# Kernel optimization log

Measured on AMD Instinct MI355X. Metric: run time of the kernel, lower is better.

## Reference

```python
import jax, jax.numpy as jnp
import numpy as np

CHUNK = 1024
HEAD_DIM = 128

def setup_inputs() -> dict:
    key = jax.random.key(0)
    k1, k2, k3 = jax.random.split(key, 3)
    B, H, S, D = 2, 16, 4096, HEAD_DIM
    q = jax.random.normal(k1, (B, H, S, D), dtype=jnp.float32)
    k = jax.random.normal(k2, (B, H, S, D), dtype=jnp.float32)
    v = jax.random.normal(k3, (B, H, S, D), dtype=jnp.float32)
    return {"q": q, "k": k, "v": v}

def reference(q, k, v):
    # Faithful to the torch module INCLUDING its masking bug: for every chunk
    # the triu mask uses diagonal=1 in chunk-local coordinates, so chunk-local
    # query row i attends only keys j<=i, i.e. only the first CHUNK keys matter.
    B, H, S, D = q.shape
    scale = D ** (-0.5)
    n = S // CHUNK
    qc = q.reshape(B, H, n, CHUNK, D)           # [B,H,n,C,D]
    kc = k[:, :, :CHUNK, :]                      # [B,H,C,D]
    vc = v[:, :, :CHUNK, :]                      # [B,H,C,D]
    scores = jnp.einsum('bhnid,bhjd->bhnij', qc, kc) * scale  # [B,H,n,C,C]
    mask = jnp.triu(jnp.ones((CHUNK, CHUNK), dtype=bool), 1)   # j > i masked
    scores = jnp.where(mask, -jnp.inf, scores)
    probs = jax.nn.softmax(scores, axis=-1)
    out = jnp.einsum('bhnij,bhjd->bhnid', probs, vc)
    return out.reshape(B, H, S, D)
```

## Files before the change

kernel.cpp:

```cpp
#include <hip/hip_runtime.h>


typedef __attribute__((ext_vector_type(8))) short bfrag_t;
typedef __attribute__((ext_vector_type(16))) float f32x16;
typedef unsigned short u16;
typedef unsigned int   u32;

#define SEQ     4096
#define SCHUNK  1024
#define HD      128
#define NTILE   16
#define TILE_E  8192

__device__ __forceinline__ u16 f2bf(float f) {
    union { float f; unsigned u; } x; x.f = f;
    unsigned r = x.u + 0x7fffu + ((x.u >> 16) & 1u);
    return (u16)(r >> 16);
}

__global__ __launch_bounds__(256)
void mea_prep(const float* __restrict__ kg, const float* __restrict__ vg,
              u16* __restrict__ wsK, u16* __restrict__ wsV)
{
    const int tid  = threadIdx.x;
    const int tile = blockIdx.x;
    const int bh = tile >> 4, kt = tile & 15;
    const long gsrc = (long)bh * SEQ * HD + (long)kt * 64 * HD;
    const long gdst = (long)tile * TILE_E;

#pragma unroll
    for (int i = 0; i < 4; ++i) {
        int oid = i * 256 + tid;
        int j = oid >> 4, s = oid & 15;
        const float* kp = kg + gsrc + j * HD + s * 8;
        float4 a = *(const float4*)kp;
        float4 b = *(const float4*)(kp + 4);
        bfrag_t f;
        f[0]=f2bf(a.x); f[1]=f2bf(a.y); f[2]=f2bf(a.z); f[3]=f2bf(a.w);
        f[4]=f2bf(b.x); f[5]=f2bf(b.y); f[6]=f2bf(b.z); f[7]=f2bf(b.w);
        *(bfrag_t*)(wsK + gdst + j * 128 + ((s ^ (j & 15)) * 8)) = f;
    }
#pragma unroll
    for (int i = 0; i < 4; ++i) {
        int oid = i * 256 + tid;
        int jo = oid >> 7, d = oid & 127;
        const float* vp = vg + gsrc + jo * 8 * HD + d;
        bfrag_t f;
#pragma unroll
        for (int jj = 0; jj < 8; ++jj) f[jj] = f2bf(vp[jj * HD]);
        int d2 = d >> 1;
        int S  = (jo + ((d & 1) << 3)) ^ (d2 & 15);
        *(bfrag_t*)(wsV + gdst + d2 * 128 + S * 8) = f;
    }
}

__device__ __forceinline__ void gll16(const u16* g, u16* l) {
    __builtin_amdgcn_global_load_lds((const __attribute__((address_space(1))) u32*)g,
                                     (__attribute__((address_space(3))) u32*)l, 16, 0, 0);
}

__device__ __forceinline__ float tsum16(const f32x16& p) {
    float a0 = (p[0] + p[1]) + (p[2] + p[3]);
    float a1 = (p[4] + p[5]) + (p[6] + p[7]);
    float a2 = (p[8] + p[9]) + (p[10] + p[11]);
    float a3 = (p[12] + p[13]) + (p[14] + p[15]);
    return (a0 + a1) + (a2 + a3);
}

__device__ __forceinline__ void sm_cvt(f32x16& s, float& lsum, bfrag_t* pf) {
#pragma unroll
    for (int r = 0; r < 16; ++r) s[r] = exp2f(s[r]);
    lsum += tsum16(s);
    u32 W[8];
#pragma unroll
    for (int t2 = 0; t2 < 8; ++t2)
        asm("v_cvt_pk_bf16_f32 %0, %1, %2"
            : "=v"(W[t2]) : "v"(s[2 * t2]), "v"(s[2 * t2 + 1]));
#pragma unroll
    for (int u2 = 0; u2 < 2; ++u2) {
        u32 x0 = W[4 * u2 + 0], y0 = W[4 * u2 + 2];
        u32 x1 = W[4 * u2 + 1], y1 = W[4 * u2 + 3];
        asm("v_permlane32_swap_b32 %0, %1" : "+v"(x0), "+v"(y0));
        asm("v_permlane32_swap_b32 %0, %1" : "+v"(x1), "+v"(y1));
        union { u32 w[4]; bfrag_t f; } cvt;
        cvt.w[0] = x0; cvt.w[1] = x1; cvt.w[2] = y0; cvt.w[3] = y1;
        pf[u2] = cvt.f;
    }
}

__global__ __launch_bounds__(512, 2)
void mea_main(const float* __restrict__ qg, const u16* __restrict__ wsK,
              const u16* __restrict__ wsV, float* __restrict__ og)
{
    __shared__ __align__(16) u16 K_s[2][TILE_E];
    __shared__ __align__(16) u16 V_s[2][TILE_E];

    const int tid  = threadIdx.x;
    const int lane = tid & 63;
    const int wv   = tid >> 6;
    const int c31  = lane & 31;
    const int hi   = lane >> 5;
    const int ch   = wv & 3;
    const int h    = wv >> 2;

    const int x   = blockIdx.x & 7;
    const int idx = blockIdx.x >> 3;
    const int bh  = x * 4 + (idx & 3);
    const int p   = idx >> 2;

    const long bhrow = (long)bh * SEQ + (long)ch * SCHUNK + (long)h * 32;
    const u16* Kb = wsK + (long)bh * NTILE * TILE_E;
    const u16* Vb = wsV + (long)bh * NTILE * TILE_E;
    const int so   = wv * 1024 + lane * 8;
    const int ldsb = wv * 1024;
    const float qs = 0.12751723f;

#pragma unroll
    for (int c = 0; c < 2; ++c) {
        gll16(Kb + so + c * 512, &K_s[0][ldsb + c * 512]);
        gll16(Vb + so + c * 512, &V_s[0][ldsb + c * 512]);
    }

    int cur = 0;
    for (int seg = 0; seg < 2; ++seg) {
        const int qt = seg ? p : (15 - p);
        const int nt = qt + 1;
        const long rowbase = bhrow + (long)qt * 64;

        bfrag_t qf[8];
        {
            const float* qp = qg + (rowbase + c31) * HD + hi * 8;
#pragma unroll
            for (int ks = 0; ks < 8; ++ks) {
                float4 a = *(const float4*)(qp + ks * 16);
                float4 b = *(const float4*)(qp + ks * 16 + 4);
                bfrag_t f;
                f[0]=f2bf(a.x*qs); f[1]=f2bf(a.y*qs); f[2]=f2bf(a.z*qs); f[3]=f2bf(a.w*qs);
                f[4]=f2bf(b.x*qs); f[5]=f2bf(b.y*qs); f[6]=f2bf(b.z*qs); f[7]=f2bf(b.w*qs);
                qf[ks] = f;
            }
        }

        f32x16 oacc[4];
#pragma unroll
        for (int d = 0; d < 4; ++d)
#pragma unroll
            for (int i = 0; i < 16; ++i) oacc[d][i] = 0.f;
        float lsum = 0.f;

        for (int kt = 0; kt < nt; ++kt) {
            __syncthreads();

            if (kt + 1 < nt) {
                const long tb = (long)(kt + 1) * TILE_E;
#pragma unroll
                for (int c = 0; c < 2; ++c) {
                    gll16(Kb + tb + so + c * 512, &K_s[cur ^ 1][ldsb + c * 512]);
                    gll16(Vb + tb + so + c * 512, &V_s[cur ^ 1][ldsb + c * 512]);
                }
            } else if (seg == 0) {
#pragma unroll
                for (int c = 0; c < 2; ++c) {
                    gll16(Kb + so + c * 512, &K_s[cur ^ 1][ldsb + c * 512]);
                    gll16(Vb + so + c * 512, &V_s[cur ^ 1][ldsb + c * 512]);
                }
            }

            const bool diag = (kt == nt - 1);
            const bool do1  = !(diag && h == 0);
            bfrag_t pfA[2], pfB[2];

            {
                f32x16 s;
#pragma unroll
                for (int i = 0; i < 16; ++i) s[i] = 0.f;
                const u16* krow = &K_s[cur][c31 * 128];
                __builtin_amdgcn_s_setprio(1);
#pragma unroll
                for (int ks = 0; ks < 8; ++ks) {
                    int slot = (ks * 2 + hi) ^ (c31 & 15);
                    bfrag_t kf = *(const bfrag_t*)(krow + slot * 8);
                    s = __builtin_amdgcn_mfma_f32_32x32x16_bf16(kf, qf[ks], s, 0, 0, 0);
                }
                __builtin_amdgcn_s_setprio(0);
                if (diag && h == 0) {
#pragma unroll
                    for (int r = 0; r < 16; ++r) {
                        int crow = (r & 3) + 8 * (r >> 2) + 4 * hi;
                        if (crow > c31) s[r] = -1e30f;
                    }
                }
                sm_cvt(s, lsum, pfA);
            }
            if (do1) {
                f32x16 s;
#pragma unroll
                for (int i = 0; i < 16; ++i) s[i] = 0.f;
                const u16* krow = &K_s[cur][(32 + c31) * 128];
                __builtin_amdgcn_s_setprio(1);
#pragma unroll
                for (int ks = 0; ks < 8; ++ks) {
                    int slot = (ks * 2 + hi) ^ (c31 & 15);
                    bfrag_t kf = *(const bfrag_t*)(krow + slot * 8);
                    s = __builtin_amdgcn_mfma_f32_32x32x16_bf16(kf, qf[ks], s, 0, 0, 0);
                }
                __builtin_amdgcn_s_setprio(0);
                if (diag) {
#pragma unroll
                    for (int r = 0; r < 16; ++r) {
                        int crow = (r & 3) + 8 * (r >> 2) + 4 * hi;
                        if (crow > c31) s[r] = -1e30f;
                    }
                }
                sm_cvt(s, lsum, pfB);
            }

            __builtin_amdgcn_s_setprio(1);
#pragma unroll
            for (int dg = 0; dg < 4; ++dg) {
                const int d  = dg * 32 + c31;
                const int d2 = d >> 1;
                const u16* vrow = &V_s[cur][d2 * 128];
#pragma unroll
                for (int jsl = 0; jsl < 2; ++jsl) {
                    int S = ((jsl * 2 + hi) + ((d & 1) << 3)) ^ (d2 & 15);
                    bfrag_t vf = *(const bfrag_t*)(vrow + S * 8);
                    oacc[dg] = __builtin_amdgcn_mfma_f32_32x32x16_bf16(vf, pfA[jsl], oacc[dg], 0, 0, 0);
                }
                if (do1) {
#pragma unroll
                    for (int jsl = 0; jsl < 2; ++jsl) {
                        int S = ((jsl + 2) * 2 + hi + ((d & 1) << 3)) ^ (d2 & 15);
                        bfrag_t vf = *(const bfrag_t*)(vrow + S * 8);
                        oacc[dg] = __builtin_amdgcn_mfma_f32_32x32x16_bf16(vf, pfB[jsl], oacc[dg], 0, 0, 0);
                    }
                }
            }
            __builtin_amdgcn_s_setprio(0);

            cur ^= 1;
        }

        lsum += __shfl_xor(lsum, 32);
        float inv = 1.f / lsum;
#pragma unroll
        for (int dg = 0; dg < 4; ++dg) {
#pragma unroll
            for (int rq = 0; rq < 4; ++rq) {
                float4 v;
                v.x = oacc[dg][rq * 4 + 0] * inv;
                v.y = oacc[dg][rq * 4 + 1] * inv;
                v.z = oacc[dg][rq * 4 + 2] * inv;
                v.w = oacc[dg][rq * 4 + 3] * inv;
                *(float4*)(og + (rowbase + c31) * HD + dg * 32 + rq * 8 + hi * 4) = v;
            }
        }
    }
}

extern "C" void kernel_launch(void* const* d_in, const int* in_sizes, int n_in,
                              void* d_out, int out_size, void* d_ws, size_t ws_size,
                              hipStream_t stream)
{
    (void)in_sizes; (void)n_in; (void)out_size; (void)ws_size;
    const float* q = (const float*)d_in[0];
    const float* k = (const float*)d_in[1];
    const float* v = (const float*)d_in[2];
    float* o = (float*)d_out;
    u16* wsK = (u16*)d_ws;
    u16* wsV = wsK + (size_t)32 * NTILE * TILE_E;
    mea_prep<<<dim3(512), dim3(256), 0, stream>>>(k, v, wsK, wsV);
    mea_main<<<dim3(256), dim3(512), 0, stream>>>(q, wsK, wsV, o);
}
```

Before: 75.85 us.

## Software-pipeline PV matmul one tile behind QK with triple-buffered V

Result: no change. 76.88 us (+1.4%).

```diff
diff --git a/kernel.cpp b/kernel.cpp
--- a/kernel.cpp
+++ b/kernel.cpp
@@ -93,7 +93,7 @@
               const u16* __restrict__ wsV, float* __restrict__ og)
 {
     __shared__ __align__(16) u16 K_s[2][TILE_E];
-    __shared__ __align__(16) u16 V_s[2][TILE_E];
+    __shared__ __align__(16) u16 V_s[3][TILE_E];
 
     const int tid  = threadIdx.x;
     const int lane = tid & 63;
@@ -121,7 +121,8 @@
         gll16(Vb + so + c * 512, &V_s[0][ldsb + c * 512]);
     }
 
-    int cur = 0;
+    int cur = 0, slCur = 0;
+
     for (int seg = 0; seg < 2; ++seg) {
         const int qt = seg ? p : (15 - p);
         const int nt = qt + 1;
@@ -148,7 +149,12 @@
             for (int i = 0; i < 16; ++i) oacc[d][i] = 0.f;
         float lsum = 0.f;
 
+        bfrag_t pfO[4];
+        int slPrev = slCur;
+        bool havePrev = false;
+
         for (int kt = 0; kt < nt; ++kt) {
+            const int slNext = (slCur == 2) ? 0 : slCur + 1;
             __syncthreads();
 
             if (kt + 1 < nt) {
@@ -156,90 +162,105 @@
 #pragma unroll
                 for (int c = 0; c < 2; ++c) {
                     gll16(Kb + tb + so + c * 512, &K_s[cur ^ 1][ldsb + c * 512]);
-                    gll16(Vb + tb + so + c * 512, &V_s[cur ^ 1][ldsb + c * 512]);
+                    gll16(Vb + tb + so + c * 512, &V_s[slNext][ldsb + c * 512]);
                 }
             } else if (seg == 0) {
 #pragma unroll
                 for (int c = 0; c < 2; ++c) {
                     gll16(Kb + so + c * 512, &K_s[cur ^ 1][ldsb + c * 512]);
-                    gll16(Vb + so + c * 512, &V_s[cur ^ 1][ldsb + c * 512]);
+                    gll16(Vb + so + c * 512, &V_s[slNext][ldsb + c * 512]);
                 }
             }
 
             const bool diag = (kt == nt - 1);
             const bool do1  = !(diag && h == 0);
-            bfrag_t pfA[2], pfB[2];
-
+            f32x16 s0, s1;
+
+            __builtin_amdgcn_s_setprio(1);
             {
-                f32x16 s;
-#pragma unroll
-                for (int i = 0; i < 16; ++i) s[i] = 0.f;
+#pragma unroll
+                for (int i = 0; i < 16; ++i) s0[i] = 0.f;
                 const u16* krow = &K_s[cur][c31 * 128];
-                __builtin_amdgcn_s_setprio(1);
 #pragma unroll
                 for (int ks = 0; ks < 8; ++ks) {
                     int slot = (ks * 2 + hi) ^ (c31 & 15);
                     bfrag_t kf = *(const bfrag_t*)(krow + slot * 8);
-                    s = __builtin_amdgcn_mfma_f32_32x32x16_bf16(kf, qf[ks], s, 0, 0, 0);
-                }
-                __builtin_amdgcn_s_setprio(0);
-                if (diag && h == 0) {
-#pragma unroll
-                    for (int r = 0; r < 16; ++r) {
-                        int crow = (r & 3) + 8 * (r >> 2) + 4 * hi;
-                        if (crow > c31) s[r] = -1e30f;
-                    }
-                }
-                sm_cvt(s, lsum, pfA);
+                    s0 = __builtin_amdgcn_mfma_f32_32x32x16_bf16(kf, qf[ks], s0, 0, 0, 0);
+                }
             }
             if (do1) {
-                f32x16 s;
-#pragma unroll
-                for (int i = 0; i < 16; ++i) s[i] = 0.f;
+#pragma unroll
+                for (int i = 0; i < 16; ++i) s1[i] = 0.f;
                 const u16* krow = &K_s[cur][(32 + c31) * 128];
-                __builtin_amdgcn_s_setprio(1);
 #pragma unroll
                 for (int ks = 0; ks < 8; ++ks) {
                     int slot = (ks * 2 + hi) ^ (c31 & 15);
                     bfrag_t kf = *(const bfrag_t*)(krow + slot * 8);
-                    s = __builtin_amdgcn_mfma_f32_32x32x16_bf16(kf, qf[ks], s, 0, 0, 0);
-                }
-                __builtin_amdgcn_s_setprio(0);
+                    s1 = __builtin_amdgcn_mfma_f32_32x32x16_bf16(kf, qf[ks], s1, 0, 0, 0);
+                }
+            }
+
+            if (havePrev) {
+#pragma unroll
+                for (int dg = 0; dg < 4; ++dg) {
+                    const int d  = dg * 32 + c31;
+                    const int d2 = d >> 1;
+                    const u16* vrow = &V_s[slPrev][d2 * 128];
+#pragma unroll
+                    for (int jsl = 0; jsl < 4; ++jsl) {
+                        int S = ((jsl * 2 + hi) + ((d & 1) << 3)) ^ (d2 & 15);
+                        bfrag_t vf = *(const bfrag_t*)(vrow + S * 8);
+                        oacc[dg] = __builtin_amdgcn_mfma_f32_32x32x16_bf16(vf, pfO[jsl], oacc[dg], 0, 0, 0);
+                    }
+                }
+            }
+            __builtin_amdgcn_s_setprio(0);
+
+            if (diag && h == 0) {
+#pragma unroll
+                for (int r = 0; r < 16; ++r) {
+                    int crow = (r & 3) + 8 * (r >> 2) + 4 * hi;
+                    if (crow > c31) s0[r] = -1e30f;
+                }
+            }
+            sm_cvt(s0, lsum, &pfO[0]);
+            if (do1) {
                 if (diag) {
 #pragma unroll
                     for (int r = 0; r < 16; ++r) {
                         int crow = (r & 3) + 8 * (r >> 2) + 4 * hi;
-                        if (crow > c31) s[r] = -1e30f;
+                        if (crow > c31) s1[r] = -1e30f;
                     }
                 }
-                sm_cvt(s, lsum, pfB);
-            }
-
-            __builtin_amdgcn_s_setprio(1);
-#pragma unroll
-            for (int dg = 0; dg < 4; ++dg) {
-                const int d  = dg * 32 + c31;
-                const int d2 = d >> 1;
-                const u16* vrow = &V_s[cur][d2 * 128];
-#pragma unroll
-                for (int jsl = 0; jsl < 2; ++jsl) {
+                sm_cvt(s1, lsum, &pfO[2]);
+            }
+
+            havePrev = true;
+            slPrev = slCur; slCur = slNext; cur ^= 1;
+        }
+
+        __builtin_amdgcn_s_setprio(1);
+#pragma unroll
+        for (int dg = 0; dg < 4; ++dg) {
+            const int d  = dg * 32 + c31;
+            const int d2 = d >> 1;
+            const u16* vrow = &V_s[slPrev][d2 * 128];
+#pragma unroll
+            for (int jsl = 0; jsl < 2; ++jsl) {
+                int S = ((jsl * 2 + hi) + ((d & 1) << 3)) ^ (d2 & 15);
+                bfrag_t vf = *(const bfrag_t*)(vrow + S * 8);
+                oacc[dg] = __builtin_amdgcn_mfma_f32_32x32x16_bf16(vf, pfO[jsl], oacc[dg], 0, 0, 0);
+            }
+            if (h) {
+#pragma unroll
+                for (int jsl = 2; jsl < 4; ++jsl) {
                     int S = ((jsl * 2 + hi) + ((d & 1) << 3)) ^ (d2 & 15);
                     bfrag_t vf = *(const bfrag_t*)(vrow + S * 8);
-                    oacc[dg] = __builtin_amdgcn_mfma_f32_32x32x16_bf16(vf, pfA[jsl], oacc[dg], 0, 0, 0);
-                }
-                if (do1) {
-#pragma unroll
-                    for (int jsl = 0; jsl < 2; ++jsl) {
-                        int S = ((jsl + 2) * 2 + hi + ((d & 1) << 3)) ^ (d2 & 15);
-                        bfrag_t vf = *(const bfrag_t*)(vrow + S * 8);
-                        oacc[dg] = __builtin_amdgcn_mfma_f32_32x32x16_bf16(vf, pfB[jsl], oacc[dg], 0, 0, 0);
-                    }
-                }
-            }
-            __builtin_amdgcn_s_setprio(0);
-
-            cur ^= 1;
-        }
+                    oacc[dg] = __builtin_amdgcn_mfma_f32_32x32x16_bf16(vf, pfO[jsl], oacc[dg], 0, 0, 0);
+                }
+            }
+        }
+        __builtin_amdgcn_s_setprio(0);
 
         lsum += __shfl_xor(lsum, 32);
         float inv = 1.f / lsum;
```
